# Optimization experiments

Measured on AMD Instinct MI355X. Metric: run time of the kernel, lower is better.

The kernel has to match this reference:

```python
import jax, jax.numpy as jnp
import numpy as np

B, S, D, H = 8, 1024, 1024, 16
DK = D // H
NEG = -1e9


def setup_inputs() -> dict:
    key = jax.random.key(0)
    ks = jax.random.split(key, 11)
    s = 1.0 / np.sqrt(D)
    inp = {
        "query": jax.random.normal(ks[0], (B, S, D), jnp.float32),
        "key": jax.random.normal(ks[1], (B, S, D), jnp.float32),
        "value": jax.random.normal(ks[2], (B, S, D), jnp.float32),
        "mask": jnp.tril(jnp.ones((S, S), jnp.int32))[None, None],  # causal [1,1,S,S]
        "w_q": jax.random.normal(ks[3], (D, D), jnp.float32) * s,
        "b_q": jnp.zeros((D,), jnp.float32),
        "w_k": jax.random.normal(ks[4], (D, D), jnp.float32) * s,
        "b_k": jnp.zeros((D,), jnp.float32),
        "w_v": jax.random.normal(ks[5], (D, D), jnp.float32) * s,
        "b_v": jnp.zeros((D,), jnp.float32),
        "w_o": jax.random.normal(ks[6], (D, D), jnp.float32) * s,
        "b_o": jnp.zeros((D,), jnp.float32),
    }
    return inp


def reference(query, key, value, mask, w_q, b_q, w_k, b_k, w_v, b_v, w_o, b_o):
    # projections; weights stored as [in, out] (torch Linear applies x @ W.T; here
    # we use x @ W which is the same math with W = torch_W.T)
    def proj(x, w, b):
        # [B,S,D] -> [B,H,S,DK]
        y = x @ w + b
        return y.reshape(B, S, H, DK).transpose(0, 2, 1, 3)

    q = proj(query, w_q, b_q)
    k = proj(key, w_k, b_k)
    v = proj(value, w_v, b_v)

    scores = jnp.einsum("bhqd,bhkd->bhqk", q, k) / jnp.sqrt(jnp.float32(DK))
    scores = jnp.where(mask == 0, jnp.float32(NEG), scores)
    probs = jax.nn.softmax(scores, axis=-1)
    # dropout: eval mode (identity) for deterministic reference
    ctx = jnp.einsum("bhqk,bhkd->bhqd", probs, v)
    ctx = ctx.transpose(0, 2, 1, 3).reshape(B, S, D)
    return ctx @ w_o + b_o
```

## Files before the change

### kernel.cpp

```cpp
#include <hip/hip_runtime.h>

#define B_ 8
#define S_ 1024
#define D_ 1024
#define H_ 16
#define DK_ 64
#define M_ (B_ * S_)
#define NEGINF -1e38f

typedef __bf16 bf16_t;
typedef __bf16 bf16x8 __attribute__((ext_vector_type(8)));
typedef float f32x4 __attribute__((ext_vector_type(4)));
typedef unsigned int u32;

__device__ inline f32x4 mfma_bf16(bf16x8 a, bf16x8 b, f32x4 c) {
    return __builtin_amdgcn_mfma_f32_16x16x32_bf16(a, b, c, 0, 0, 0);
}

typedef const __attribute__((address_space(1))) u32* gas1_t;
typedef __attribute__((address_space(3))) u32* las3_t;
__device__ inline void gl_lds16(const void* g, void* l) {
    __builtin_amdgcn_global_load_lds((gas1_t)g, (las3_t)l, 16, 0, 0);
}

__device__ inline bf16x8 load8(const bf16_t* p) { return *(const bf16x8*)p; }
__device__ inline bf16x8 load8(const float* p) {
    const f32x4 a = *(const f32x4*)p;
    const f32x4 b = *(const f32x4*)(p + 4);
    bf16x8 r;
    r[0] = (bf16_t)a[0]; r[1] = (bf16_t)a[1];
    r[2] = (bf16_t)a[2]; r[3] = (bf16_t)a[3];
    r[4] = (bf16_t)b[0]; r[5] = (bf16_t)b[1];
    r[6] = (bf16_t)b[2]; r[7] = (bf16_t)b[3];
    return r;
}
__device__ inline void store_elem(bf16_t* Y, size_t i, float v) { Y[i] = (bf16_t)v; }
__device__ inline void store_elem(float* Y, size_t i, float v) { Y[i] = v; }

__global__ __launch_bounds__(256) void transpose4(
    const float* __restrict__ i0, const float* __restrict__ i1,
    const float* __restrict__ i2, const float* __restrict__ i3,
    bf16_t* __restrict__ o0, bf16_t* __restrict__ o1,
    bf16_t* __restrict__ o2, bf16_t* __restrict__ o3) {
    const float* ins[4] = {i0, i1, i2, i3};
    bf16_t* outs[4] = {o0, o1, o2, o3};
    const float* in = ins[blockIdx.z];
    bf16_t* out = outs[blockIdx.z];
    __shared__ __align__(16) bf16_t t[32][33];
    const int n0 = blockIdx.x * 32, k0 = blockIdx.y * 32;
    const int tx = threadIdx.x;
    for (int i = threadIdx.y; i < 32; i += 8)
        t[i][tx] = (bf16_t)in[(size_t)(k0 + i) * D_ + n0 + tx];
    __syncthreads();
    for (int i = threadIdx.y; i < 32; i += 8)
        out[(size_t)(n0 + i) * D_ + k0 + tx] = t[tx][i];
}

__global__ __launch_bounds__(256) void cvt_bf16(const float* __restrict__ in,
                                                bf16_t* __restrict__ out,
                                                int n8) {
    const int i = blockIdx.x * 256 + threadIdx.x;
    if (i < n8) *(bf16x8*)(out + (size_t)i * 8) = load8(in + (size_t)i * 8);
}

template <int MODE, typename TX, typename TY>
__global__ __launch_bounds__(256) void gemm_bt(
    const TX* __restrict__ X, const bf16_t* __restrict__ Wt,
    const float* __restrict__ bias, TY* __restrict__ Y, float scale) {
    __shared__ __align__(16) bf16_t As[128 * 64];
    __shared__ __align__(16) bf16_t Bs[128 * 64];
    const int tid = threadIdx.x;
    const int lane = tid & 63, wave = tid >> 6;
    const int ln = lane & 15, quad = lane >> 4;
    const int wm = (wave & 1) * 64, wn = (wave >> 1) * 64;
    const int m0 = blockIdx.x * 128, n0 = blockIdx.y * 128;

    const int srow = tid >> 3;
    const int sch = tid & 7;
    const int swc = sch ^ (srow & 7);

    const TX* pa = X + (size_t)(m0 + srow) * D_ + swc * 8;
    const bf16_t* pb = Wt + (size_t)(n0 + srow) * D_ + swc * 8;

    f32x4 acc[4][4] = {};
    for (int k0 = 0; k0 < D_; k0 += 64) {
        if constexpr (sizeof(TX) == 2) {
#pragma unroll
            for (int i = 0; i < 4; i++)
                gl_lds16(pa + (size_t)(i * 32) * D_ + k0,
                         As + i * 2048 + wave * 512);
        } else {
#pragma unroll
            for (int i = 0; i < 4; i++)
                *(bf16x8*)(As + (srow + i * 32) * 64 + sch * 8) =
                    load8(X + (size_t)(m0 + srow + i * 32) * D_ + k0 + swc * 8);
        }
#pragma unroll
        for (int i = 0; i < 4; i++)
            gl_lds16(pb + (size_t)(i * 32) * D_ + k0,
                     Bs + i * 2048 + wave * 512);
        __syncthreads();
#pragma unroll
        for (int kq = 0; kq < 2; kq++) {
            bf16x8 af[4], bfr[4];
            const int slot = ((kq * 4 + quad) ^ (ln & 7)) * 8;
#pragma unroll
            for (int mt = 0; mt < 4; mt++)
                af[mt] = *(const bf16x8*)(As + (wm + mt * 16 + ln) * 64 + slot);
#pragma unroll
            for (int nt = 0; nt < 4; nt++)
                bfr[nt] = *(const bf16x8*)(Bs + (wn + nt * 16 + ln) * 64 + slot);
#pragma unroll
            for (int mt = 0; mt < 4; mt++)
#pragma unroll
                for (int nt = 0; nt < 4; nt++)
                    acc[mt][nt] = mfma_bf16(af[mt], bfr[nt], acc[mt][nt]);
        }
        __syncthreads();
    }

#pragma unroll
    for (int mt = 0; mt < 4; mt++) {
#pragma unroll
        for (int nt = 0; nt < 4; nt++) {
#pragma unroll
            for (int r = 0; r < 4; r++) {
                const int m = m0 + wm + mt * 16 + quad * 4 + r;
                const int n = n0 + wn + nt * 16 + ln;
                const float v = (acc[mt][nt][r] + bias[n]) * scale;
                size_t idx;
                if (MODE == 0) {
                    idx = (size_t)m * D_ + n;
                } else {
                    const int b = m >> 10, s = m & 1023;
                    const int h = n >> 6, d = n & 63;
                    if (MODE == 1)
                        idx = ((size_t)(b * H_ + h) * S_ + s) * DK_ + d;
                    else
                        idx = ((size_t)(b * H_ + h) * DK_ + d) * S_ + s;
                }
                store_elem(Y, idx, v);
            }
        }
    }
}

__global__ __launch_bounds__(256, 4) void MaskedMultiHeadAttention_90709709291709_kernel(
    const bf16_t* __restrict__ Q, const bf16_t* __restrict__ K,
    const bf16_t* __restrict__ Vt, bf16_t* __restrict__ ctx) {
    __shared__ __align__(16) bf16_t Ks[64 * 64];
    __shared__ __align__(16) bf16_t Vs[64 * 64];
    __shared__ __align__(16) bf16_t pbuf[4][32 * 64];

    const int bh = blockIdx.x;
    const int j = 7 - (int)blockIdx.y;
    const int tid = threadIdx.x;
    const int lane = tid & 63, wave = tid >> 6;
    const int ln = lane & 15, quad = lane >> 4;

    const bf16_t* Qb = Q + (size_t)bh * S_ * DK_;
    const bf16_t* Kb = K + (size_t)bh * S_ * DK_;
    const bf16_t* Vb = Vt + (size_t)bh * DK_ * S_;
    const int b = bh >> 4, h = bh & 15;

    bf16x8 ones8;
#pragma unroll
    for (int i = 0; i < 8; i++) ones8[i] = (bf16_t)1.0f;

    const int qb = j * 128;
    const int wq = qb + wave * 32;
    bf16_t* pb = pbuf[wave];

    bf16x8 qf[2][2];
#pragma unroll
    for (int mi = 0; mi < 2; mi++)
#pragma unroll
        for (int kk = 0; kk < 2; kk++)
            qf[mi][kk] = *(const bf16x8*)(
                Qb + (size_t)(wq + mi * 16 + ln) * DK_ + kk * 32 + quad * 8);

    f32x4 o[2][4] = {};
    f32x4 ol[2] = {};

    const int r8 = lane >> 3;
    const int sc = (lane & 7) ^ r8;

    const int kend = qb + 128;
    for (int kt = 0; kt < kend; kt += 64) {
#pragma unroll
        for (int i = 0; i < 2; i++) {
            const int row = (wave * 2 + i) * 8 + r8;
            gl_lds16(Kb + (size_t)(kt + row) * DK_ + sc * 8,
                     Ks + (wave * 2 + i) * 512);
            gl_lds16(Vb + (size_t)row * S_ + kt + sc * 8,
                     Vs + (wave * 2 + i) * 512);
        }
        __syncthreads();

        if (kt <= wq + 31) {
#pragma unroll
            for (int nt = 0; nt < 4; nt++) {
                const bf16_t* kp = Ks + (nt * 16 + ln) * 64;
                const bf16x8 kf0 = *(const bf16x8*)(kp + ((quad ^ (ln & 7)) * 8));
                const bf16x8 kf1 =
                    *(const bf16x8*)(kp + (((4 + quad) ^ (ln & 7)) * 8));
#pragma unroll
                for (int mi = 0; mi < 2; mi++) {
                    f32x4 a = {-16.f, -16.f, -16.f, -16.f};
                    a = mfma_bf16(qf[mi][0], kf0, a);
                    a = mfma_bf16(qf[mi][1], kf1, a);
                    const bool needmask = (kt + 63) > (wq + mi * 16);
#pragma unroll
                    for (int r = 0; r < 4; r++) {
                        const int row = wq + mi * 16 + quad * 4 + r;
                        const int prow = mi * 16 + quad * 4 + r;
                        float v = a[r];
                        if (needmask && (kt + nt * 16 + ln > row)) v = NEGINF;
                        const float p = __builtin_amdgcn_exp2f(v);
                        const int col = nt * 16 + ln;
                        pb[prow * 64 + (((col >> 3) ^ (prow & 7)) * 8) +
                           (col & 7)] = (bf16_t)p;
                    }
                }
            }

            bf16x8 pf[2][2];
#pragma unroll
            for (int mi = 0; mi < 2; mi++)
#pragma unroll
                for (int kk = 0; kk < 2; kk++)
                    pf[mi][kk] = *(const bf16x8*)(
                        pb + (mi * 16 + ln) * 64 +
                        (((kk * 4 + quad) ^ (ln & 7)) * 8));
#pragma unroll
            for (int mi = 0; mi < 2; mi++) {
                ol[mi] = mfma_bf16(pf[mi][0], ones8, ol[mi]);
                ol[mi] = mfma_bf16(pf[mi][1], ones8, ol[mi]);
            }
#pragma unroll
            for (int dk = 0; dk < 4; dk++) {
                const bf16_t* vp = Vs + (dk * 16 + ln) * 64;
                const bf16x8 vf0 = *(const bf16x8*)(vp + ((quad ^ (ln & 7)) * 8));
                const bf16x8 vf1 =
                    *(const bf16x8*)(vp + (((4 + quad) ^ (ln & 7)) * 8));
#pragma unroll
                for (int mi = 0; mi < 2; mi++) {
                    o[mi][dk] = mfma_bf16(pf[mi][0], vf0, o[mi][dk]);
                    o[mi][dk] = mfma_bf16(pf[mi][1], vf1, o[mi][dk]);
                }
            }
        }
        __syncthreads();
    }

#pragma unroll
    for (int mi = 0; mi < 2; mi++)
#pragma unroll
        for (int r = 0; r < 4; r++) {
            const float inv = 1.f / ol[mi][r];
            const int row = wq + mi * 16 + quad * 4 + r;
            const size_t base = ((size_t)b * S_ + row) * D_ + h * DK_;
#pragma unroll
            for (int dk = 0; dk < 4; dk++)
                ctx[base + dk * 16 + ln] = (bf16_t)(o[mi][dk][r] * inv);
        }
}

__global__ __launch_bounds__(256) void copy16(const f32x4* __restrict__ src,
                                              f32x4* __restrict__ dst, int n4) {
    const int i = blockIdx.x * 256 + threadIdx.x;
    if (i < n4) dst[i] = src[i];
}

extern "C" void kernel_launch(void* const* d_in, const int* in_sizes, int n_in,
                              void* d_out, int out_size, void* d_ws,
                              size_t ws_size, hipStream_t stream) {
    const float* query = (const float*)d_in[0];
    const float* key = (const float*)d_in[1];
    const float* value = (const float*)d_in[2];
    const float* w_q = (const float*)d_in[4];
    const float* b_q = (const float*)d_in[5];
    const float* w_k = (const float*)d_in[6];
    const float* b_k = (const float*)d_in[7];
    const float* w_v = (const float*)d_in[8];
    const float* b_v = (const float*)d_in[9];
    const float* w_o = (const float*)d_in[10];
    const float* b_o = (const float*)d_in[11];

    bf16_t* ws = (bf16_t*)d_ws;
    const size_t M8 = (size_t)M_ * D_;
    bf16_t* Qw = ws;
    bf16_t* Kw = ws + M8;
    bf16_t* Vw = ws + 2 * M8;
    bf16_t* wtq = ws + 3 * M8;
    bf16_t* wtk = wtq + (size_t)D_ * D_;
    bf16_t* wtv = wtk + (size_t)D_ * D_;
    bf16_t* wto = wtv + (size_t)D_ * D_;

    bf16_t* Xb = (bf16_t*)d_out;

    const size_t need_direct = (4 * M8 + 4 * (size_t)D_ * D_) * sizeof(bf16_t);
    const bool direct = ws_size >= need_direct;
    bf16_t* Cw = direct ? (ws + 3 * M8 + 4 * (size_t)D_ * D_)
                        : (bf16_t*)d_out;
    float* Yw = direct ? (float*)d_out : (float*)ws;

    transpose4<<<dim3(32, 32, 4), dim3(32, 8, 1), 0, stream>>>(
        w_q, w_k, w_v, w_o, wtq, wtk, wtv, wto);

    const dim3 gg(M_ / 128, D_ / 128, 1);
    const int n8 = (int)(M8 / 8);
    const dim3 gc((n8 + 255) / 256, 1, 1);
    const float qscale = 0.125f * 1.4426950408889634f;

    cvt_bf16<<<gc, 256, 0, stream>>>(query, Xb, n8);
    gemm_bt<1><<<gg, 256, 0, stream>>>(Xb, wtq, b_q, Qw, qscale);
    cvt_bf16<<<gc, 256, 0, stream>>>(key, Xb, n8);
    gemm_bt<1><<<gg, 256, 0, stream>>>(Xb, wtk, b_k, Kw, 1.0f);
    cvt_bf16<<<gc, 256, 0, stream>>>(value, Xb, n8);
    gemm_bt<2><<<gg, 256, 0, stream>>>(Xb, wtv, b_v, Vw, 1.0f);

    MaskedMultiHeadAttention_90709709291709_kernel<<<dim3(B_ * H_, 8, 1), 256,
                                                     0, stream>>>(Qw, Kw, Vw,
                                                                  Cw);

    gemm_bt<0><<<gg, 256, 0, stream>>>(Cw, wto, b_o, Yw, 1.0f);
    if (!direct) {
        const int n4 = (int)((M8 * 4) / 16);
        copy16<<<dim3((n4 + 255) / 256), 256, 0, stream>>>((const f32x4*)Yw,
                                                           (f32x4*)d_out, n4);
    }
}
```

Before: 328.0 us.

## Double-buffer GEMM LDS tiles and keep attention probabilities in registers

The projection GEMM now uses two LDS buffers per operand and issues the next k-tile's loads before computing on the current one. This is meant to hide global-to-LDS latency behind the MFMAs, at the cost of doubling shared memory (64KB per block), which can lower occupancy. The attention kernel computes S^T via swapped MFMA operands and permutes the K rows on load so the probability fragments land directly in the register layout needed for the PV MFMA. That removes the per-wave LDS round-trip for P, but the mask index mapping becomes intricate and a mistake there would be a correctness risk.

```diff
diff --git a/kernel.cpp b/kernel.cpp
--- a/kernel.cpp
+++ b/kernel.cpp
@@ -67,8 +67,8 @@
 __global__ __launch_bounds__(256) void gemm_bt(
     const TX* __restrict__ X, const bf16_t* __restrict__ Wt,
     const float* __restrict__ bias, TY* __restrict__ Y, float scale) {
-    __shared__ __align__(16) bf16_t As[128 * 64];
-    __shared__ __align__(16) bf16_t Bs[128 * 64];
+    __shared__ __align__(16) bf16_t As[2][128 * 64];
+    __shared__ __align__(16) bf16_t Bs[2][128 * 64];
     const int tid = threadIdx.x;
     const int lane = tid & 63, wave = tid >> 6;
     const int ln = lane & 15, quad = lane >> 4;
@@ -82,34 +82,43 @@
     const TX* pa = X + (size_t)(m0 + srow) * D_ + swc * 8;
     const bf16_t* pb = Wt + (size_t)(n0 + srow) * D_ + swc * 8;
 
-    f32x4 acc[4][4] = {};
-    for (int k0 = 0; k0 < D_; k0 += 64) {
+    auto stage = [&](int d, int k0) {
         if constexpr (sizeof(TX) == 2) {
 #pragma unroll
             for (int i = 0; i < 4; i++)
                 gl_lds16(pa + (size_t)(i * 32) * D_ + k0,
-                         As + i * 2048 + wave * 512);
+                         As[d] + i * 2048 + wave * 512);
         } else {
 #pragma unroll
             for (int i = 0; i < 4; i++)
-                *(bf16x8*)(As + (srow + i * 32) * 64 + sch * 8) =
+                *(bf16x8*)(As[d] + (srow + i * 32) * 64 + sch * 8) =
                     load8(X + (size_t)(m0 + srow + i * 32) * D_ + k0 + swc * 8);
         }
 #pragma unroll
         for (int i = 0; i < 4; i++)
             gl_lds16(pb + (size_t)(i * 32) * D_ + k0,
-                     Bs + i * 2048 + wave * 512);
-        __syncthreads();
+                     Bs[d] + i * 2048 + wave * 512);
+    };
+
+    stage(0, 0);
+    __syncthreads();
+
+    f32x4 acc[4][4] = {};
+    int cur = 0;
+    for (int t = 0; t < 16; ++t) {
+        if (t < 15) stage(cur ^ 1, (t + 1) * 64);
 #pragma unroll
         for (int kq = 0; kq < 2; kq++) {
             bf16x8 af[4], bfr[4];
             const int slot = ((kq * 4 + quad) ^ (ln & 7)) * 8;
 #pragma unroll
             for (int mt = 0; mt < 4; mt++)
-                af[mt] = *(const bf16x8*)(As + (wm + mt * 16 + ln) * 64 + slot);
+                af[mt] =
+                    *(const bf16x8*)(As[cur] + (wm + mt * 16 + ln) * 64 + slot);
 #pragma unroll
             for (int nt = 0; nt < 4; nt++)
-                bfr[nt] = *(const bf16x8*)(Bs + (wn + nt * 16 + ln) * 64 + slot);
+                bfr[nt] =
+                    *(const bf16x8*)(Bs[cur] + (wn + nt * 16 + ln) * 64 + slot);
 #pragma unroll
             for (int mt = 0; mt < 4; mt++)
 #pragma unroll
@@ -117,6 +126,7 @@
                     acc[mt][nt] = mfma_bf16(af[mt], bfr[nt], acc[mt][nt]);
         }
         __syncthreads();
+        cur ^= 1;
     }
 
 #pragma unroll
@@ -150,7 +160,6 @@
     const bf16_t* __restrict__ Vt, bf16_t* __restrict__ ctx) {
     __shared__ __align__(16) bf16_t Ks[64 * 64];
     __shared__ __align__(16) bf16_t Vs[64 * 64];
-    __shared__ __align__(16) bf16_t pbuf[4][32 * 64];
 
     const int bh = blockIdx.x;
     const int j = 7 - (int)blockIdx.y;
@@ -169,7 +178,6 @@
 
     const int qb = j * 128;
     const int wq = qb + wave * 32;
-    bf16_t* pb = pbuf[wave];
 
     bf16x8 qf[2][2];
 #pragma unroll
@@ -189,53 +197,58 @@
     for (int kt = 0; kt < kend; kt += 64) {
 #pragma unroll
         for (int i = 0; i < 2; i++) {
-            const int row = (wave * 2 + i) * 8 + r8;
-            gl_lds16(Kb + (size_t)(kt + row) * DK_ + sc * 8,
-                     Ks + (wave * 2 + i) * 512);
-            gl_lds16(Vb + (size_t)row * S_ + kt + sc * 8,
-                     Vs + (wave * 2 + i) * 512);
+            const int g = wave * 2 + i;
+            const int krow = (g & 2) * 16 + (g & 1) * 16 + (r8 & 4) * 2 +
+                             (g & 4) + (r8 & 3);
+            gl_lds16(Kb + (size_t)(kt + krow) * DK_ + sc * 8, Ks + g * 512);
+            gl_lds16(Vb + (size_t)(g * 8 + r8) * S_ + kt + sc * 8,
+                     Vs + g * 512);
         }
         __syncthreads();
 
         if (kt <= wq + 31) {
-#pragma unroll
-            for (int nt = 0; nt < 4; nt++) {
-                const bf16_t* kp = Ks + (nt * 16 + ln) * 64;
-                const bf16x8 kf0 = *(const bf16x8*)(kp + ((quad ^ (ln & 7)) * 8));
-                const bf16x8 kf1 =
-                    *(const bf16x8*)(kp + (((4 + quad) ^ (ln & 7)) * 8));
-#pragma unroll
-                for (int mi = 0; mi < 2; mi++) {
+            bf16x8 pa[2][2];
+#pragma unroll
+            for (int mi = 0; mi < 2; mi++) {
+                f32x4 s[4];
+#pragma unroll
+                for (int nt = 0; nt < 4; nt++) {
+                    const bf16_t* kp = Ks + (nt * 16 + ln) * 64;
+                    const bf16x8 kf0 =
+                        *(const bf16x8*)(kp + ((quad ^ (ln & 7)) * 8));
+                    const bf16x8 kf1 =
+                        *(const bf16x8*)(kp + (((4 + quad) ^ (ln & 7)) * 8));
                     f32x4 a = {-16.f, -16.f, -16.f, -16.f};
-                    a = mfma_bf16(qf[mi][0], kf0, a);
-                    a = mfma_bf16(qf[mi][1], kf1, a);
-                    const bool needmask = (kt + 63) > (wq + mi * 16);
+                    a = mfma_bf16(kf0, qf[mi][0], a);
+                    a = mfma_bf16(kf1, qf[mi][1], a);
+                    s[nt] = a;
+                }
+                const int q = wq + mi * 16 + ln;
+                const bool needmask = (kt + 63) > q;
+#pragma unroll
+                for (int nt = 0; nt < 4; nt++)
 #pragma unroll
                     for (int r = 0; r < 4; r++) {
-                        const int row = wq + mi * 16 + quad * 4 + r;
-                        const int prow = mi * 16 + quad * 4 + r;
-                        float v = a[r];
-                        if (needmask && (kt + nt * 16 + ln > row)) v = NEGINF;
-                        const float p = __builtin_amdgcn_exp2f(v);
-                        const int col = nt * 16 + ln;
-                        pb[prow * 64 + (((col >> 3) ^ (prow & 7)) * 8) +
-                           (col & 7)] = (bf16_t)p;
+                        const int ktrue = kt + (nt & 1) * 32 + quad * 8 +
+                                          (nt >> 1) * 4 + r;
+                        float v = s[nt][r];
+                        if (needmask && ktrue > q) v = NEGINF;
+                        s[nt][r] = __builtin_amdgcn_exp2f(v);
                     }
+#pragma unroll
+                for (int kk = 0; kk < 2; kk++) {
+                    bf16x8 t;
+#pragma unroll
+                    for (int w = 0; w < 4; w++) {
+                        const int nts = 2 * (w >> 1) + kk;
+                        const int r0 = 2 * (w & 1);
+                        t[2 * w] = (bf16_t)s[nts][r0];
+                        t[2 * w + 1] = (bf16_t)s[nts][r0 + 1];
+                    }
+                    pa[mi][kk] = t;
                 }
-            }
-
-            bf16x8 pf[2][2];
-#pragma unroll
-            for (int mi = 0; mi < 2; mi++)
-#pragma unroll
-                for (int kk = 0; kk < 2; kk++)
-                    pf[mi][kk] = *(const bf16x8*)(
-                        pb + (mi * 16 + ln) * 64 +
-                        (((kk * 4 + quad) ^ (ln & 7)) * 8));
-#pragma unroll
-            for (int mi = 0; mi < 2; mi++) {
-                ol[mi] = mfma_bf16(pf[mi][0], ones8, ol[mi]);
-                ol[mi] = mfma_bf16(pf[mi][1], ones8, ol[mi]);
+                ol[mi] = mfma_bf16(pa[mi][0], ones8, ol[mi]);
+                ol[mi] = mfma_bf16(pa[mi][1], ones8, ol[mi]);
             }
 #pragma unroll
             for (int dk = 0; dk < 4; dk++) {
@@ -245,8 +258,8 @@
                     *(const bf16x8*)(vp + (((4 + quad) ^ (ln & 7)) * 8));
 #pragma unroll
                 for (int mi = 0; mi < 2; mi++) {
-                    o[mi][dk] = mfma_bf16(pf[mi][0], vf0, o[mi][dk]);
-                    o[mi][dk] = mfma_bf16(pf[mi][1], vf1, o[mi][dk]);
+                    o[mi][dk] = mfma_bf16(pa[mi][0], vf0, o[mi][dk]);
+                    o[mi][dk] = mfma_bf16(pa[mi][1], vf1, o[mi][dk]);
                 }
             }
         }
```

Measured after the change: 309.7 us. -5.6%, faster.
